# Performance work log

Hardware: AMD Instinct MI355X
Metric: run time of the kernel (lower is better)

Reference implementation:

```python
import jax, jax.numpy as jnp
import numpy as np

D = 1024
H = 16
HD = D // H
T = 2048
B = 2
EPS = 1e-7

def setup_inputs() -> dict:
    key = jax.random.key(0)
    ks = jax.random.split(key, 16)
    s = 0.02
    return {
        "x":  jax.random.normal(ks[0], (B, T, D), jnp.float32),
        "Wq": jax.random.normal(ks[1], (D, D), jnp.float32) * s,
        "bq": jnp.zeros((D,), jnp.float32),
        "Wk": jax.random.normal(ks[2], (D, D), jnp.float32) * s,
        "bk": jnp.zeros((D,), jnp.float32),
        "Wv": jax.random.normal(ks[3], (D, D), jnp.float32) * s,
        "bv": jnp.zeros((D,), jnp.float32),
        "Wo": jax.random.normal(ks[4], (D, D), jnp.float32) * s,
        "bo": jnp.zeros((D,), jnp.float32),
        "W1": jax.random.normal(ks[5], (D, 4 * D), jnp.float32) * s,
        "b1": jnp.zeros((4 * D,), jnp.float32),
        "W2": jax.random.normal(ks[6], (4 * D, D), jnp.float32) * s,
        "b2": jnp.zeros((D,), jnp.float32),
        "g1": jnp.ones((D,), jnp.float32),
        "be1": jnp.zeros((D,), jnp.float32),
        "g2": jnp.ones((D,), jnp.float32),
        "be2": jnp.zeros((D,), jnp.float32),
    }

def layer_norm(x, gamma, beta):
    mu = jnp.mean(x, axis=-1, keepdims=True)
    var = jnp.mean(jnp.square(x - mu), axis=-1, keepdims=True)  # biased var
    return (x - mu) / jnp.sqrt(var + EPS) * gamma + beta

def attention(x, Wq, bq, Wk, bk, Wv, bv, Wo, bo):
    b, t, d = x.shape
    q = (x @ Wq + bq).reshape(b, t, H, HD).transpose(0, 2, 1, 3)  # [B,H,T,HD]
    k = (x @ Wk + bk).reshape(b, t, H, HD).transpose(0, 2, 1, 3)
    v = (x @ Wv + bv).reshape(b, t, H, HD).transpose(0, 2, 1, 3)
    scores = jnp.einsum("bhqd,bhkd->bhqk", q, k) / np.sqrt(HD).astype(np.float32)
    causal = jnp.tril(jnp.ones((t, t), bool))
    scores = jnp.where(causal, scores, -jnp.inf)
    attn = jax.nn.softmax(scores, axis=-1)
    out = jnp.einsum("bhqk,bhkd->bhqd", attn, v)
    out = out.transpose(0, 2, 1, 3).reshape(b, t, d)
    return out @ Wo + bo

def reference(x, Wq, bq, Wk, bk, Wv, bv, Wo, bo, W1, b1, W2, b2, g1, be1, g2, be2):
    x = x + attention(layer_norm(x, g1, be1), Wq, bq, Wk, bk, Wv, bv, Wo, bo)
    h = layer_norm(x, g2, be2)
    x = x + (jax.nn.relu(h @ W1 + b1) @ W2 + b2)
    return x
```

## Files before the change

### kernel.cpp

```cpp
#include <hip/hip_runtime.h>
#include <hip/hip_bf16.h>

#define Dm 1024
#define Hn 16
#define HDm 64
#define Tm 2048
#define Bm 2
#define MR (Bm*Tm)
#define SQK 3072

typedef __attribute__((ext_vector_type(8))) short bfrag8;
typedef __attribute__((ext_vector_type(4))) float floatx4;

__device__ __forceinline__ float bf2f(ushort u){
  union { unsigned int i; float f; } c; c.i = ((unsigned int)u)<<16; return c.f;
}
__device__ __forceinline__ ushort f2bf(float f){
  unsigned int u = __float_as_uint(f);
  u += 0x7fffu + ((u>>16)&1u);
  return (ushort)(u>>16);
}
__device__ __forceinline__ void gl2lds16(const ushort* g, ushort* l){
  __builtin_amdgcn_global_load_lds(
    (const __attribute__((address_space(1))) unsigned int*)g,
    (__attribute__((address_space(3))) unsigned int*)l,
    16, 0, 0);
}
__device__ __forceinline__ int is_f32(const unsigned int* g1w){
  return *g1w == 0x3F800000u;
}

#define POFF0 (1ul*524288)
#define POFF1 (9ul*524288)
#define POFF2 (25ul*524288)
#define POFF3 (73ul*524288)

__global__ __launch_bounds__(256) void prep_vec(const void* bq, const void* bk, const void* bv,
                                                const void* bo, const void* b1, const void* b2,
                                                const void* g1, const void* be1,
                                                const void* g2, const void* be2,
                                                float* __restrict__ dst){
  int i = blockIdx.x*256 + threadIdx.x;
  if (i >= 13312) return;
  int f = is_f32((const unsigned int*)g1);
  const void* src; int off;
  if      (i < 1024)  { src = bq;  off = i; }
  else if (i < 2048)  { src = bk;  off = i-1024; }
  else if (i < 3072)  { src = bv;  off = i-2048; }
  else if (i < 4096)  { src = bo;  off = i-3072; }
  else if (i < 8192)  { src = b1;  off = i-4096; }
  else if (i < 9216)  { src = b2;  off = i-8192; }
  else if (i < 10240) { src = g1;  off = i-9216; }
  else if (i < 11264) { src = be1; off = i-10240; }
  else if (i < 12288) { src = g2;  off = i-11264; }
  else                { src = be2; off = i-12288; }
  dst[i] = f ? ((const float*)src)[off] : bf2f(((const ushort*)src)[off]);
}

__device__ __forceinline__ void transpose_body(const void* src, ushort* dst,
                                               int K, int N, int f32){
  __shared__ ushort s[32][33];
  int bx = blockIdx.x, by = blockIdx.y;
  int tx = threadIdx.x, ty = threadIdx.y;
#pragma unroll
  for(int r=0;r<4;r++){
    size_t gi = (size_t)(by*32+ty+8*r)*N + bx*32+tx;
    s[ty+8*r][tx] = f32 ? f2bf(((const float*)src)[gi]) : ((const ushort*)src)[gi];
  }
  __syncthreads();
#pragma unroll
  for(int r=0;r<4;r++)
    dst[(size_t)(bx*32+ty+8*r)*K + by*32+tx] = s[tx][ty+8*r];
}
__global__ __launch_bounds__(256) void transpose_cast(const void* __restrict__ src,
                                                      ushort* __restrict__ dst,
                                                      int K, int N, const unsigned int* g1w){
  transpose_body(src, dst, K, N, is_f32(g1w));
}
__global__ __launch_bounds__(256) void transpose_qkvo(const void* Wq, const void* Wk,
                                                      const void* Wv, const void* Wo,
                                                      ushort* __restrict__ Wqkvt,
                                                      ushort* __restrict__ Wot,
                                                      const unsigned int* g1w){
  int z = blockIdx.z;
  const void* src = (z==0)?Wq:(z==1)?Wk:(z==2)?Wv:Wo;
  ushort* dst = (z<3) ? (Wqkvt + (size_t)z*1024*1024) : Wot;
  transpose_body(src, dst, 1024, 1024, is_f32(g1w));
}

__global__ __launch_bounds__(256) void vtrans(const ushort* __restrict__ qkv,
                                              ushort* __restrict__ vt){
  __shared__ ushort s[32][33];
  int bhz = blockIdx.z;
  int bx = blockIdx.x;
  int by = blockIdx.y;
  int tx = threadIdx.x, ty = threadIdx.y;
  int b = bhz>>4, h = bhz&15;
  const ushort* src = qkv + (size_t)b*Tm*SQK + 2048 + h*64;
#pragma unroll
  for(int r=0;r<4;r++)
    s[ty+8*r][tx] = src[(size_t)(bx*32+ty+8*r)*SQK + by*32+tx];
  __syncthreads();
  ushort* dst = vt + (size_t)bhz*HDm*Tm;
#pragma unroll
  for(int r=0;r<4;r++)
    dst[(size_t)(by*32+ty+8*r)*Tm + bx*32+tx] = s[tx][ty+8*r];
}

template<int MODE>
__global__ __launch_bounds__(256) void ln_kernel(const void* __restrict__ xin,
                                                 const float* __restrict__ g,
                                                 const float* __restrict__ be,
                                                 ushort* __restrict__ out,
                                                 const unsigned int* g1w){
  int row = blockIdx.x;
  int tid = threadIdx.x;
  size_t base = (size_t)row*Dm + tid*4;
  float v[4];
  bool f32in = (MODE==1) || (MODE==0 && is_f32(g1w));
  if (f32in){
    const float4 t = *(const float4*)((const float*)xin + base);
    v[0]=t.x; v[1]=t.y; v[2]=t.z; v[3]=t.w;
  } else {
    ushort4 t = *(const ushort4*)((const ushort*)xin + base);
    v[0]=bf2f(t.x); v[1]=bf2f(t.y); v[2]=bf2f(t.z); v[3]=bf2f(t.w);
  }
  float s  = v[0]+v[1]+v[2]+v[3];
  float s2 = v[0]*v[0]+v[1]*v[1]+v[2]*v[2]+v[3]*v[3];
#pragma unroll
  for(int o=1;o<64;o<<=1){
    s  += __shfl_xor(s,  o, 64);
    s2 += __shfl_xor(s2, o, 64);
  }
  __shared__ float red[8];
  int wv = tid>>6;
  if ((tid&63)==0){ red[wv]=s; red[wv+4]=s2; }
  __syncthreads();
  s  = red[0]+red[1]+red[2]+red[3];
  s2 = red[4]+red[5]+red[6]+red[7];
  float mu  = s  * (1.0f/Dm);
  float var = s2 * (1.0f/Dm) - mu*mu;
  float rstd = rsqrtf(var + 1e-7f);
  float4 gg = *(const float4*)(g  + tid*4);
  float4 bb = *(const float4*)(be + tid*4);
  ushort4 o4;
  o4.x = f2bf((v[0]-mu)*rstd*gg.x+bb.x);
  o4.y = f2bf((v[1]-mu)*rstd*gg.y+bb.y);
  o4.z = f2bf((v[2]-mu)*rstd*gg.z+bb.z);
  o4.w = f2bf((v[3]-mu)*rstd*gg.w+bb.w);
  *(ushort4*)(out + base) = o4;
}

#define BKt 64
enum { E_BF16=0, E_RELU=1, E_OPROJ=2, E_FINALB=3, E_PARTB=4, E_PARTB4=5 };

template<int EPI>
__global__ __launch_bounds__(512,2) void gemm256(const ushort* __restrict__ A, int lda,
                                                 const ushort* __restrict__ Bt, int ldb,
                                                 const float* __restrict__ bias,
                                                 void* __restrict__ Cout, int ldc,
                                                 int Ki,
                                                 const unsigned int* g1w){
  __shared__ ushort lds[65536];
  int tid = threadIdx.x;
  int lin = blockIdx.x;
  int xcd = lin&7, pos = lin>>3;
  int bm, bn, zid = 0;
  if (EPI==E_BF16){        bm=(xcd&3)*4+(pos&3);  bn=(xcd>>2)*6+(pos>>2); }
  else if (EPI==E_RELU){   bm=(xcd&3)*4+(pos&3);  bn=(xcd>>2)*8+(pos>>2); }
  else if (EPI==E_PARTB4){ zid=xcd>>1; bm=(xcd&1)*8+(pos>>2); bn=pos&3; }
  else {                   zid=xcd&1;  bm=(xcd>>1)*4+(pos>>2); bn=pos&3; }
  int wv = tid>>6, lane = tid&63;
  int quad = lane>>4, l16 = lane&15;
  int wm = (wv>>2)*128, wn = (wv&3)*64;
  int rl = lane>>3;
  int cs = ((lane&7)^rl)*8;
  const ushort* Aptr = A  + (size_t)bm*256*lda + (size_t)zid*Ki;
  const ushort* Bptr = Bt + (size_t)bn*256*ldb + (size_t)zid*Ki;
  floatx4 acc[8][4] = {};
  bfrag8 afr[4][2], bfr[4][2];
  const int NI = Ki>>7;

  auto STG = [&](ushort* dst, const ushort* g, int ld){
    gl2lds16(&g[(size_t)(wv*16+rl)*ld + cs],   dst + (wv*16)*64);
    gl2lds16(&g[(size_t)(wv*16+8+rl)*ld + cs], dst + (wv*16+8)*64);
  };
  auto LD8 = [&](const ushort* base, int r, int G)->bfrag8{
    return *(const bfrag8*)&base[r*64 + ((G ^ (r&7))<<3)];
  };
#define BAR256 __builtin_amdgcn_s_barrier()
#define LGKM0  do{ asm volatile("s_waitcnt lgkmcnt(0)" ::: "memory"); __builtin_amdgcn_sched_barrier(0);}while(0)
#define MM256(a_,b_,c_) c_ = __builtin_amdgcn_mfma_f32_16x16x32_bf16(a_,b_,c_,0,0,0)

  STG(lds+32768,      Bptr,                    ldb);
  STG(lds+32768+8192, Bptr+(size_t)128*ldb,    ldb);
  STG(lds,            Aptr,                    lda);
  STG(lds+8192,       Aptr+(size_t)128*lda,    lda);
  STG(lds+49152,      Bptr+64,                 ldb);
  STG(lds+49152+8192, Bptr+(size_t)128*ldb+64, ldb);
  STG(lds+16384,      Aptr+64,                 lda);
  asm volatile("s_waitcnt vmcnt(6)" ::: "memory");
  BAR256;

  for(int i=0;i<NI;i++){
    bool nl = (i < NI-1);
    int kc = i*128;
#pragma unroll
    for(int m=0;m<4;m++){ int r=wm+m*16+l16;
      afr[m][0]=LD8(lds, r, quad);  afr[m][1]=LD8(lds, r, 4|quad); }
#pragma unroll
    for(int j=0;j<4;j++){ int r=wn+j*16+l16;
      bfr[j][0]=LD8(lds+32768, r, quad); bfr[j][1]=LD8(lds+32768, r, 4|quad); }
    STG(lds+16384+8192, Aptr+(size_t)128*lda + kc+64, lda);
    BAR256; LGKM0;
    __builtin_amdgcn_s_setprio(1);
#pragma unroll
    for(int m=0;m<4;m++)
#pragma unroll
      for(int j=0;j<2;j++){ MM256(afr[m][0],bfr[j][0],acc[m][j]); MM256(afr[m][1],bfr[j][1],acc[m][j]); }
    __builtin_amdgcn_s_setprio(0);
    BAR256;
    if(nl) STG(lds+32768, Bptr + kc+128, ldb);
    BAR256;
    __builtin_amdgcn_s_setprio(1);
#pragma unroll
    for(int m=0;m<4;m++)
#pragma unroll
      for(int j=2;j<4;j++){ MM256(afr[m][0],bfr[j][0],acc[m][j]); MM256(afr[m][1],bfr[j][1],acc[m][j]); }
    __builtin_amdgcn_s_setprio(0);
    BAR256;
#pragma unroll
    for(int m=0;m<4;m++){ int r=wm+(4+m)*16+l16;
      afr[m][0]=LD8(lds, r, quad);  afr[m][1]=LD8(lds, r, 4|quad); }
    if(nl) STG(lds+32768+8192, Bptr+(size_t)128*ldb + kc+128, ldb);
    BAR256; LGKM0;
    __builtin_amdgcn_s_setprio(1);
#pragma unroll
    for(int m=0;m<4;m++)
#pragma unroll
      for(int j=2;j<4;j++){ MM256(afr[m][0],bfr[j][0],acc[4+m][j]); MM256(afr[m][1],bfr[j][1],acc[4+m][j]); }
    __builtin_amdgcn_s_setprio(0);
    BAR256;
    if(nl) STG(lds, Aptr + kc+128, lda);
    BAR256;
    __builtin_amdgcn_s_setprio(1);
#pragma unroll
    for(int m=0;m<4;m++)
#pragma unroll
      for(int j=0;j<2;j++){ MM256(afr[m][0],bfr[j][0],acc[4+m][j]); MM256(afr[m][1],bfr[j][1],acc[4+m][j]); }
    __builtin_amdgcn_s_setprio(0);
    if(nl) asm volatile("s_waitcnt vmcnt(6)" ::: "memory");
    else   asm volatile("s_waitcnt vmcnt(0)" ::: "memory");
    BAR256;
#pragma unroll
    for(int m=0;m<4;m++){ int r=wm+m*16+l16;
      afr[m][0]=LD8(lds+16384, r, quad);  afr[m][1]=LD8(lds+16384, r, 4|quad); }
#pragma unroll
    for(int j=0;j<4;j++){ int r=wn+j*16+l16;
      bfr[j][0]=LD8(lds+49152, r, quad); bfr[j][1]=LD8(lds+49152, r, 4|quad); }
    if(nl) STG(lds+8192, Aptr+(size_t)128*lda + kc+128, lda);
    BAR256; LGKM0;
    __builtin_amdgcn_s_setprio(1);
#pragma unroll
    for(int m=0;m<4;m++)
#pragma unroll
      for(int j=0;j<2;j++){ MM256(afr[m][0],bfr[j][0],acc[m][j]); MM256(afr[m][1],bfr[j][1],acc[m][j]); }
    __builtin_amdgcn_s_setprio(0);
    BAR256;
    if(nl) STG(lds+49152, Bptr + kc+192, ldb);
    BAR256;
    __builtin_amdgcn_s_setprio(1);
#pragma unroll
    for(int m=0;m<4;m++)
#pragma unroll
      for(int j=2;j<4;j++){ MM256(afr[m][0],bfr[j][0],acc[m][j]); MM256(afr[m][1],bfr[j][1],acc[m][j]); }
    __builtin_amdgcn_s_setprio(0);
    BAR256;
#pragma unroll
    for(int m=0;m<4;m++){ int r=wm+(4+m)*16+l16;
      afr[m][0]=LD8(lds+16384, r, quad);  afr[m][1]=LD8(lds+16384, r, 4|quad); }
    if(nl) STG(lds+49152+8192, Bptr+(size_t)128*ldb + kc+192, ldb);
    BAR256; LGKM0;
    __builtin_amdgcn_s_setprio(1);
#pragma unroll
    for(int m=0;m<4;m++)
#pragma unroll
      for(int j=2;j<4;j++){ MM256(afr[m][0],bfr[j][0],acc[4+m][j]); MM256(afr[m][1],bfr[j][1],acc[4+m][j]); }
    __builtin_amdgcn_s_setprio(0);
    BAR256;
    if(nl) STG(lds+16384, Aptr + kc+192, lda);
    BAR256;
    __builtin_amdgcn_s_setprio(1);
#pragma unroll
    for(int m=0;m<4;m++)
#pragma unroll
      for(int j=0;j<2;j++){ MM256(afr[m][0],bfr[j][0],acc[4+m][j]); MM256(afr[m][1],bfr[j][1],acc[4+m][j]); }
    __builtin_amdgcn_s_setprio(0);
    if(nl){ asm volatile("s_waitcnt vmcnt(6)" ::: "memory"); }
    BAR256;
  }

  ushort* part = (ushort*)Cout;
  if (EPI==E_PARTB)  part += (size_t)zid*MR*1024;
  if (EPI==E_PARTB4) part += (zid==0?POFF0 : zid==1?POFF1 : zid==2?POFF2 : POFF3);
#pragma unroll
  for(int i2=0;i2<8;i2++){
    int gr = bm*256 + wm + i2*16 + quad*4;
#pragma unroll
    for(int j=0;j<4;j++){
      int gc = bn*256 + wn + j*16 + l16;
      float bb = (EPI==E_PARTB || EPI==E_PARTB4) ? 0.0f : bias[gc];
#pragma unroll
      for(int rg=0; rg<4; rg++){
        size_t idx = (size_t)(gr+rg)*ldc + gc;
        float val = acc[i2][j][rg] + bb;
        if (EPI==E_RELU) part[idx] = f2bf(val>0.0f?val:0.0f);
        else             part[idx] = f2bf(val);
      }
    }
  }
#undef BAR256
#undef LGKM0
#undef MM256
}

__global__ __launch_bounds__(256) void ffn2_reduce(const ushort* __restrict__ p0,
                                                   const ushort* __restrict__ p1,
                                                   const float* __restrict__ bias,
                                                   const ushort* __restrict__ resid,
                                                   void* __restrict__ out,
                                                   const unsigned int* g1w){
  int e = (blockIdx.x*256 + threadIdx.x)*4;
  ushort4 a = *(const ushort4*)&p0[e];
  ushort4 b = *(const ushort4*)&p1[e];
  ushort4 r = *(const ushort4*)&resid[e];
  float4 bb = *(const float4*)&bias[e & 1023];
  float v0 = bf2f(a.x)+bf2f(b.x)+bb.x+bf2f(r.x);
  float v1 = bf2f(a.y)+bf2f(b.y)+bb.y+bf2f(r.y);
  float v2 = bf2f(a.z)+bf2f(b.z)+bb.z+bf2f(r.z);
  float v3 = bf2f(a.w)+bf2f(b.w)+bb.w+bf2f(r.w);
  if (is_f32(g1w)){
    float4 o = {v0,v1,v2,v3};
    *(float4*)((float*)out + e) = o;
  } else {
    ushort4 o = {f2bf(v0),f2bf(v1),f2bf(v2),f2bf(v3)};
    *(ushort4*)((ushort*)out + e) = o;
  }
}

__global__ __launch_bounds__(256) void ffn2_reduce4(const ushort* __restrict__ pb,
                                                    const float* __restrict__ bias,
                                                    const ushort* __restrict__ resid,
                                                    void* __restrict__ out,
                                                    const unsigned int* g1w){
  int e = (blockIdx.x*256 + threadIdx.x)*4;
  ushort4 a = *(const ushort4*)&pb[POFF0 + e];
  ushort4 b = *(const ushort4*)&pb[POFF1 + e];
  ushort4 c = *(const ushort4*)&pb[POFF2 + e];
  ushort4 d = *(const ushort4*)&pb[POFF3 + e];
  ushort4 r = *(const ushort4*)&resid[e];
  float4 bb = *(const float4*)&bias[e & 1023];
  float v0 = bf2f(a.x)+bf2f(b.x)+bf2f(c.x)+bf2f(d.x)+bb.x+bf2f(r.x);
  float v1 = bf2f(a.y)+bf2f(b.y)+bf2f(c.y)+bf2f(d.y)+bb.y+bf2f(r.y);
  float v2 = bf2f(a.z)+bf2f(b.z)+bf2f(c.z)+bf2f(d.z)+bb.z+bf2f(r.z);
  float v3 = bf2f(a.w)+bf2f(b.w)+bf2f(c.w)+bf2f(d.w)+bb.w+bf2f(r.w);
  if (is_f32(g1w)){
    float4 o = {v0,v1,v2,v3};
    *(float4*)((float*)out + e) = o;
  } else {
    ushort4 o = {f2bf(v0),f2bf(v1),f2bf(v2),f2bf(v3)};
    *(ushort4*)((ushort*)out + e) = o;
  }
}

template<int EPI>
__global__ __launch_bounds__(128) void gemm64_bt(const ushort* __restrict__ A, int lda,
                                                 const ushort* __restrict__ Bt, int ldb,
                                                 const float* __restrict__ bias,
                                                 const void*   __restrict__ resid,
                                                 void* __restrict__ Cout, int ldc,
                                                 int Ki,
                                                 const unsigned int* g1w){
  __shared__ ushort As[64*BKt];
  __shared__ ushort Bs[64*BKt];
  int tid = threadIdx.x;
  int id = blockIdx.x;
  int xcd = id&7, sdec = id>>3;
  int bn = sdec&15, bm = (sdec>>4)*8 + xcd;
  int wv = tid>>6, lane = tid&63;
  int quad = lane>>4, l16 = lane&15;
  int wm = wv*32;
  floatx4 acc[2][4] = {};
  const ushort* Aptr = A  + (size_t)bm*64*lda;
  const ushort* Bptr = Bt + (size_t)bn*64*ldb;
  int rl = lane>>3;
  int cs = ((lane&7) ^ rl)*8;

  for(int k0=0; k0<Ki; k0+=BKt){
    __syncthreads();
#pragma unroll
    for(int c=0;c<4;c++){
      gl2lds16(&Aptr[(size_t)(wv*32 + c*8 + rl)*lda + k0 + cs], &As[(wv*32 + c*8)*BKt]);
      gl2lds16(&Bptr[(size_t)(wv*32 + c*8 + rl)*ldb + k0 + cs], &Bs[(wv*32 + c*8)*BKt]);
    }
    __syncthreads();
#pragma unroll
    for(int f=0;f<2;f++){
      int sw = (((f<<2)|quad) ^ (l16&7))*8;
      bfrag8 a[2], b[4];
#pragma unroll
      for(int i=0;i<2;i++) a[i] = *(const bfrag8*)&As[(wm+i*16+l16)*BKt + sw];
#pragma unroll
      for(int j=0;j<4;j++) b[j] = *(const bfrag8*)&Bs[(j*16+l16)*BKt + sw];
#pragma unroll
      for(int i=0;i<2;i++)
#pragma unroll
        for(int j=0;j<4;j++)
          acc[i][j] = __builtin_amdgcn_mfma_f32_16x16x32_bf16(a[i], b[j], acc[i][j], 0,0,0);
    }
  }

  int f32 = is_f32(g1w);
#pragma unroll
  for(int i=0;i<2;i++){
    int gr = bm*64 + wm + i*16 + quad*4;
#pragma unroll
    for(int j=0;j<4;j++){
      int gc = bn*64 + j*16 + l16;
      float bb = bias[gc];
#pragma unroll
      for(int rg=0; rg<4; rg++){
        size_t idx = (size_t)(gr+rg)*ldc + gc;
        float val = acc[i][j][rg] + bb;
        if (EPI==E_OPROJ){
          float r = f32 ? ((const float*)resid)[idx] : bf2f(((const ushort*)resid)[idx]);
          ((ushort*)Cout)[idx] = f2bf(val + r);
        } else {
          float r = bf2f(((const ushort*)resid)[idx]);
          if (f32) ((float*)Cout)[idx] = val + r;
          else     ((ushort*)Cout)[idx] = f2bf(val + r);
        }
      }
    }
  }
}

#define PSTR2 72

__global__ __launch_bounds__(256) void attn_mfma(const ushort* __restrict__ qkv,
                                                 const ushort* __restrict__ vt,
                                                 ushort* __restrict__ pn0,
                                                 ushort* __restrict__ pn1,
                                                 float* __restrict__ den0,
                                                 float* __restrict__ den1){
  __shared__ ushort Ks[64*64];
  __shared__ ushort Vs[64*64];
  __shared__ ushort Ps[64*PSTR2];
  int id = blockIdx.x;
  int xcd = id&7, s = id>>3;
  int v = s>>6;
  int hb = (s>>4)&3;
  int p = s&15;
  int h = xcd + 8*(hb&1), b = hb>>1;
  int tid = threadIdx.x;
  int wv = tid>>6, lane = tid&63;
  int quad = lane>>4, l16 = lane&15;
  const ushort* qbase = qkv + (size_t)b*Tm*SQK + h*HDm;
  const ushort* kbase = qbase + Dm;
  const ushort* vtb   = vt + (size_t)(b*Hn+h)*HDm*Tm;
  size_t obase = (size_t)b*Tm*Dm + (size_t)h*HDm;
  int rl = lane>>3;
  int cs = ((lane&7) ^ rl)*8;
  ushort* pn = v ? pn1 : pn0;
  float* den = v ? den1 : den0;

  for(int tt=0; tt<2; tt++){
    int qt = tt ? (31-p) : p;
    int r0 = tt ? (1-v) : v;

    int qrow = qt*64 + wv*16 + l16;
    bfrag8 aq[2];
#pragma unroll
    for(int f=0;f<2;f++){
      bfrag8 raw = *(const bfrag8*)&qbase[(size_t)qrow*SQK + f*32 + quad*8];
#pragma unroll
      for(int e=0;e<8;e++) aq[f][e] = (short)f2bf(bf2f((ushort)raw[e])*0.125f);
    }

    floatx4 oacc[4] = {};
    float lacc = 0.0f;
    int qglob = qt*64 + wv*16 + l16;

    for(int r=r0; r<=qt; r+=2){
      __syncthreads();
#pragma unroll
      for(int c=0;c<2;c++){
        int kr0 = wv*16 + c*8;
        gl2lds16(&kbase[(size_t)(r*64 + kr0 + rl)*SQK + cs], &Ks[kr0*64]);
        gl2lds16(&vtb[(size_t)(kr0 + rl)*Tm + r*64 + cs], &Vs[kr0*64]);
      }
      __syncthreads();

      floatx4 sv[4];
#pragma unroll
      for(int j=0;j<4;j++){
        int kr = j*16 + l16;
        int k7 = kr & 7;
        bfrag8 k0 = *(const bfrag8*)&Ks[kr*64 + ((quad     ^ k7)*8)];
        bfrag8 k1 = *(const bfrag8*)&Ks[kr*64 + (((4|quad) ^ k7)*8)];
        floatx4 z = {0.0f,0.0f,0.0f,0.0f};
        z = __builtin_amdgcn_mfma_f32_16x16x32_bf16(k0, aq[0], z, 0,0,0);
        z = __builtin_amdgcn_mfma_f32_16x16x32_bf16(k1, aq[1], z, 0,0,0);
        sv[j] = z;
      }
      if (r == qt){
#pragma unroll
        for(int j=0;j<4;j++){
          int gk0 = r*64 + j*16 + quad*4;
#pragma unroll
          for(int rg=0;rg<4;rg++)
            if (gk0 + rg > qglob) sv[j][rg] = -1.0e30f;
        }
      }

#pragma unroll
      for(int j=0;j<4;j++){
        float p0 = __expf(sv[j][0]);
        float p1 = __expf(sv[j][1]);
        float p2 = __expf(sv[j][2]);
        float p3 = __expf(sv[j][3]);
        lacc += (p0+p1)+(p2+p3);
        unsigned w0, w1;
        asm("v_cvt_pk_bf16_f32 %0, %1, %2" : "=v"(w0) : "v"(p0), "v"(p1));
        asm("v_cvt_pk_bf16_f32 %0, %1, %2" : "=v"(w1) : "v"(p2), "v"(p3));
        uint2 ww; ww.x = w0; ww.y = w1;
        *(uint2*)&Ps[(wv*16 + l16)*PSTR2 + j*16 + quad*4] = ww;
      }

      bfrag8 ap[2];
#pragma unroll
      for(int c=0;c<2;c++)
        ap[c] = *(const bfrag8*)&Ps[(wv*16 + l16)*PSTR2 + c*32 + quad*8];

#pragma unroll
      for(int j=0;j<4;j++){
        int dr = j*16 + l16;
        int d7 = dr & 7;
#pragma unroll
        for(int c=0;c<2;c++){
          bfrag8 bv = *(const bfrag8*)&Vs[dr*64 + (((c*4+quad) ^ d7)*8)];
          oacc[j] = __builtin_amdgcn_mfma_f32_16x16x32_bf16(ap[c], bv, oacc[j], 0,0,0);
        }
      }
    }

    lacc += __shfl_xor(lacc, 16, 64);
    lacc += __shfl_xor(lacc, 32, 64);
    if (lane < 16)
      den[(size_t)(b*Hn+h)*Tm + qt*64 + wv*16 + lane] = lacc;

#pragma unroll
    for(int j=0;j<4;j++)
#pragma unroll
      for(int rg=0;rg<4;rg++){
        int t = qt*64 + wv*16 + quad*4 + rg;
        pn[obase + (size_t)t*Dm + j*16 + l16] = f2bf(oacc[j][rg]);
      }
  }
}

__global__ __launch_bounds__(256) void attn_combine(const ushort* __restrict__ n1,
                                                    const float* __restrict__ den0,
                                                    const float* __restrict__ den1,
                                                    ushort* __restrict__ n0out){
  int e = (blockIdx.x*256 + threadIdx.x)*4;
  int row = e >> 10;
  int col = e & 1023;
  int h = col >> 6;
  int b = row >> 11;
  int t = row & 2047;
  size_t di = (size_t)(b*Hn+h)*Tm + t;
  float inv = 1.0f / (den0[di] + den1[di]);
  ushort4 a = *(const ushort4*)&n0out[e];
  ushort4 c = *(const ushort4*)&n1[e];
  ushort4 o;
  o.x = f2bf((bf2f(a.x)+bf2f(c.x))*inv);
  o.y = f2bf((bf2f(a.y)+bf2f(c.y))*inv);
  o.z = f2bf((bf2f(a.z)+bf2f(c.z))*inv);
  o.w = f2bf((bf2f(a.w)+bf2f(c.w))*inv);
  *(ushort4*)&n0out[e] = o;
}

extern "C" void kernel_launch(void* const* d_in, const int* in_sizes, int n_in,
                              void* d_out, int out_size, void* d_ws, size_t ws_size,
                              hipStream_t stream) {
  const void* x   = d_in[0];
  const void* Wq  = d_in[1];
  const void* bq  = d_in[2];
  const void* Wk  = d_in[3];
  const void* bk  = d_in[4];
  const void* Wv  = d_in[5];
  const void* bv  = d_in[6];
  const void* Wo  = d_in[7];
  const void* bo  = d_in[8];
  const void* W1  = d_in[9];
  const void* b1  = d_in[10];
  const void* W2  = d_in[11];
  const void* b2  = d_in[12];
  const void* g1  = d_in[13];
  const void* be1 = d_in[14];
  const void* g2  = d_in[15];
  const void* be2 = d_in[16];
  const unsigned int* g1w = (const unsigned int*)g1;

  char* ws = (char*)d_ws;
  const size_t MB = 1024*1024;
  float*  biasf = (float*)(ws + 65536);
  float*  den0c = (float*)(ws + 256*1024);
  float*  den1c = (float*)(ws + 512*1024);
  ushort* Wqkvt = (ushort*)(ws + 1*MB);
  ushort* Wot   = (ushort*)(ws + 7*MB);
  ushort* W1t   = (ushort*)(ws + 9*MB);
  ushort* W2t   = (ushort*)(ws + 17*MB);
  ushort* p0    = (ushort*)(ws + 1*MB);
  ushort* p1    = (ushort*)(ws + 9*MB);
  ushort* ln1   = (ushort*)(ws + 25*MB);
  ushort* vtb   = (ushort*)(ws + 25*MB);
  ushort* h2    = (ushort*)(ws + 25*MB);
  ushort* qkv   = (ushort*)(ws + 33*MB);
  ushort* atb   = (ushort*)(ws + 57*MB);
  ushort* pn1b  = (ushort*)(ws + 65*MB);
  ushort* x1b   = (ushort*)(ws + 65*MB);
  ushort* h1    = (ushort*)(ws + 33*MB);

  prep_vec<<<52, 256, 0, stream>>>(bq,bk,bv,bo,b1,b2,g1,be1,g2,be2, biasf);

  dim3 tb(32,8);
  transpose_qkvo<<<dim3(32,32,4), tb, 0, stream>>>(Wq, Wk, Wv, Wo, Wqkvt, Wot, g1w);
  transpose_cast<<<dim3(128,32), tb, 0, stream>>>(W1, W1t, 1024, 4096, g1w);
  transpose_cast<<<dim3(32,128), tb, 0, stream>>>(W2, W2t, 4096, 1024, g1w);

  ln_kernel<0><<<MR, 256, 0, stream>>>(x, biasf+9216, biasf+10240, ln1, g1w);

  gemm256<E_BF16><<<192, 512, 0, stream>>>(ln1, 1024, Wqkvt, 1024, biasf, qkv, SQK, 1024, g1w);

  vtrans<<<dim3(64,2,32), tb, 0, stream>>>(qkv, vtb);

  attn_mfma<<<1024, 256, 0, stream>>>(qkv, vtb, atb, pn1b, den0c, den1c);
  attn_combine<<<4096, 256, 0, stream>>>(pn1b, den0c, den1c, atb);

  gemm64_bt<E_OPROJ><<<1024, 128, 0, stream>>>(atb, 1024, Wot, 1024, biasf+3072, x, x1b, 1024, 1024, g1w);

  ln_kernel<2><<<MR, 256, 0, stream>>>(x1b, biasf+11264, biasf+12288, h2, g1w);

  gemm256<E_RELU><<<256, 512, 0, stream>>>(h2, 1024, W1t, 1024, biasf+4096, h1, 4096, 1024, g1w);

  if (ws_size >= 82*MB){
    gemm256<E_PARTB4><<<256, 512, 0, stream>>>(h1, 4096, W2t, 4096, nullptr, d_ws, 1024, 1024, g1w);
    ffn2_reduce4<<<4096, 256, 0, stream>>>((const ushort*)d_ws, biasf+8192, x1b, d_out, g1w);
  } else {
    gemm256<E_PARTB><<<128, 512, 0, stream>>>(h1, 4096, W2t, 4096, nullptr, p0, 1024, 2048, g1w);
    ffn2_reduce<<<4096, 256, 0, stream>>>(p0, p1, biasf+8192, x1b, d_out, g1w);
  }
}
```

Baseline: 339.4 us.

## Fuse V transpose into QKV GEMM epilogue and stagger B-fragment LDS loads

```diff
diff --git a/kernel.cpp b/kernel.cpp
--- a/kernel.cpp
+++ b/kernel.cpp
@@ -88,25 +88,6 @@
   transpose_body(src, dst, 1024, 1024, is_f32(g1w));
 }
 
-__global__ __launch_bounds__(256) void vtrans(const ushort* __restrict__ qkv,
-                                              ushort* __restrict__ vt){
-  __shared__ ushort s[32][33];
-  int bhz = blockIdx.z;
-  int bx = blockIdx.x;
-  int by = blockIdx.y;
-  int tx = threadIdx.x, ty = threadIdx.y;
-  int b = bhz>>4, h = bhz&15;
-  const ushort* src = qkv + (size_t)b*Tm*SQK + 2048 + h*64;
-#pragma unroll
-  for(int r=0;r<4;r++)
-    s[ty+8*r][tx] = src[(size_t)(bx*32+ty+8*r)*SQK + by*32+tx];
-  __syncthreads();
-  ushort* dst = vt + (size_t)bhz*HDm*Tm;
-#pragma unroll
-  for(int r=0;r<4;r++)
-    dst[(size_t)(by*32+ty+8*r)*Tm + bx*32+tx] = s[tx][ty+8*r];
-}
-
 template<int MODE>
 __global__ __launch_bounds__(256) void ln_kernel(const void* __restrict__ xin,
                                                  const float* __restrict__ g,
@@ -160,6 +141,7 @@
                                                  const float* __restrict__ bias,
                                                  void* __restrict__ Cout, int ldc,
                                                  int Ki,
+                                                 ushort* __restrict__ vtout,
                                                  const unsigned int* g1w){
   __shared__ ushort lds[65536];
   int tid = threadIdx.x;
@@ -173,6 +155,7 @@
   int wv = tid>>6, lane = tid&63;
   int quad = lane>>4, l16 = lane&15;
   int wm = (wv>>2)*128, wn = (wv&3)*64;
+  int hiw = (wv>>1)&1;
   int rl = lane>>3;
   int cs = ((lane&7)^rl)*8;
   const ushort* Aptr = A  + (size_t)bm*256*lda + (size_t)zid*Ki;
@@ -209,8 +192,13 @@
     for(int m=0;m<4;m++){ int r=wm+m*16+l16;
       afr[m][0]=LD8(lds, r, quad);  afr[m][1]=LD8(lds, r, 4|quad); }
 #pragma unroll
-    for(int j=0;j<4;j++){ int r=wn+j*16+l16;
+    for(int j=0;j<2;j++){ int r=wn+j*16+l16;
       bfr[j][0]=LD8(lds+32768, r, quad); bfr[j][1]=LD8(lds+32768, r, 4|quad); }
+    if(!hiw){
+#pragma unroll
+      for(int j=2;j<4;j++){ int r=wn+j*16+l16;
+        bfr[j][0]=LD8(lds+32768, r, quad); bfr[j][1]=LD8(lds+32768, r, 4|quad); }
+    }
     STG(lds+16384+8192, Aptr+(size_t)128*lda + kc+64, lda);
     BAR256; LGKM0;
     __builtin_amdgcn_s_setprio(1);
@@ -220,8 +208,13 @@
       for(int j=0;j<2;j++){ MM256(afr[m][0],bfr[j][0],acc[m][j]); MM256(afr[m][1],bfr[j][1],acc[m][j]); }
     __builtin_amdgcn_s_setprio(0);
     BAR256;
+    if(hiw){
+#pragma unroll
+      for(int j=2;j<4;j++){ int r=wn+j*16+l16;
+        bfr[j][0]=LD8(lds+32768, r, quad); bfr[j][1]=LD8(lds+32768, r, 4|quad); }
+    }
     if(nl) STG(lds+32768, Bptr + kc+128, ldb);
-    BAR256;
+    BAR256; LGKM0;
     __builtin_amdgcn_s_setprio(1);
 #pragma unroll
     for(int m=0;m<4;m++)
@@ -256,8 +249,13 @@
     for(int m=0;m<4;m++){ int r=wm+m*16+l16;
       afr[m][0]=LD8(lds+16384, r, quad);  afr[m][1]=LD8(lds+16384, r, 4|quad); }
 #pragma unroll
-    for(int j=0;j<4;j++){ int r=wn+j*16+l16;
+    for(int j=0;j<2;j++){ int r=wn+j*16+l16;
       bfr[j][0]=LD8(lds+49152, r, quad); bfr[j][1]=LD8(lds+49152, r, 4|quad); }
+    if(!hiw){
+#pragma unroll
+      for(int j=2;j<4;j++){ int r=wn+j*16+l16;
+        bfr[j][0]=LD8(lds+49152, r, quad); bfr[j][1]=LD8(lds+49152, r, 4|quad); }
+    }
     if(nl) STG(lds+8192, Aptr+(size_t)128*lda + kc+128, lda);
     BAR256; LGKM0;
     __builtin_amdgcn_s_setprio(1);
@@ -267,8 +265,13 @@
       for(int j=0;j<2;j++){ MM256(afr[m][0],bfr[j][0],acc[m][j]); MM256(afr[m][1],bfr[j][1],acc[m][j]); }
     __builtin_amdgcn_s_setprio(0);
     BAR256;
+    if(hiw){
+#pragma unroll
+      for(int j=2;j<4;j++){ int r=wn+j*16+l16;
+        bfr[j][0]=LD8(lds+49152, r, quad); bfr[j][1]=LD8(lds+49152, r, 4|quad); }
+    }
     if(nl) STG(lds+49152, Bptr + kc+192, ldb);
-    BAR256;
+    BAR256; LGKM0;
     __builtin_amdgcn_s_setprio(1);
 #pragma unroll
     for(int m=0;m<4;m++)
@@ -310,12 +313,19 @@
     for(int j=0;j<4;j++){
       int gc = bn*256 + wn + j*16 + l16;
       float bb = (EPI==E_PARTB || EPI==E_PARTB4) ? 0.0f : bias[gc];
+      ushort4 vv;
 #pragma unroll
       for(int rg=0; rg<4; rg++){
         size_t idx = (size_t)(gr+rg)*ldc + gc;
         float val = acc[i2][j][rg] + bb;
-        if (EPI==E_RELU) part[idx] = f2bf(val>0.0f?val:0.0f);
-        else             part[idx] = f2bf(val);
+        ushort w = (EPI==E_RELU) ? f2bf(val>0.0f?val:0.0f) : f2bf(val);
+        part[idx] = w;
+        if (EPI==E_BF16) ((ushort*)&vv)[rg] = w;
+      }
+      if (EPI==E_BF16 && gc >= 2048){
+        int hh = (gc-2048)>>6, dd = (gc-2048)&63;
+        int vb = gr>>11, t0 = gr&2047;
+        *(ushort4*)&vtout[(((size_t)(vb*Hn+hh))*HDm + dd)*Tm + t0] = vv;
       }
     }
   }
@@ -624,10 +634,10 @@
   ushort* W2t   = (ushort*)(ws + 17*MB);
   ushort* p0    = (ushort*)(ws + 1*MB);
   ushort* p1    = (ushort*)(ws + 9*MB);
-  ushort* ln1   = (ushort*)(ws + 25*MB);
   ushort* vtb   = (ushort*)(ws + 25*MB);
   ushort* h2    = (ushort*)(ws + 25*MB);
   ushort* qkv   = (ushort*)(ws + 33*MB);
+  ushort* ln1   = (ushort*)(ws + 57*MB);
   ushort* atb   = (ushort*)(ws + 57*MB);
   ushort* pn1b  = (ushort*)(ws + 65*MB);
   ushort* x1b   = (ushort*)(ws + 65*MB);
@@ -642,9 +652,7 @@
 
   ln_kernel<0><<<MR, 256, 0, stream>>>(x, biasf+9216, biasf+10240, ln1, g1w);
 
-  gemm256<E_BF16><<<192, 512, 0, stream>>>(ln1, 1024, Wqkvt, 1024, biasf, qkv, SQK, 1024, g1w);
-
-  vtrans<<<dim3(64,2,32), tb, 0, stream>>>(qkv, vtb);
+  gemm256<E_BF16><<<192, 512, 0, stream>>>(ln1, 1024, Wqkvt, 1024, biasf, qkv, SQK, 1024, vtb, g1w);
 
   attn_mfma<<<1024, 256, 0, stream>>>(qkv, vtb, atb, pn1b, den0c, den1c);
   attn_combine<<<4096, 256, 0, stream>>>(pn1b, den0c, den1c, atb);
@@ -653,13 +661,13 @@
 
   ln_kernel<2><<<MR, 256, 0, stream>>>(x1b, biasf+11264, biasf+12288, h2, g1w);
 
-  gemm256<E_RELU><<<256, 512, 0, stream>>>(h2, 1024, W1t, 1024, biasf+4096, h1, 4096, 1024, g1w);
+  gemm256<E_RELU><<<256, 512, 0, stream>>>(h2, 1024, W1t, 1024, biasf+4096, h1, 4096, 1024, nullptr, g1w);
 
   if (ws_size >= 82*MB){
-    gemm256<E_PARTB4><<<256, 512, 0, stream>>>(h1, 4096, W2t, 4096, nullptr, d_ws, 1024, 1024, g1w);
+    gemm256<E_PARTB4><<<256, 512, 0, stream>>>(h1, 4096, W2t, 4096, nullptr, d_ws, 1024, 1024, nullptr, g1w);
     ffn2_reduce4<<<4096, 256, 0, stream>>>((const ushort*)d_ws, biasf+8192, x1b, d_out, g1w);
   } else {
-    gemm256<E_PARTB><<<128, 512, 0, stream>>>(h1, 4096, W2t, 4096, nullptr, p0, 1024, 2048, g1w);
+    gemm256<E_PARTB><<<128, 512, 0, stream>>>(h1, 4096, W2t, 4096, nullptr, p0, 1024, 2048, nullptr, g1w);
     ffn2_reduce<<<4096, 256, 0, stream>>>(p0, p1, biasf+8192, x1b, d_out, g1w);
   }
 }
```

New measurement: 334.1 us. Within noise of the previous version (-1.5%).
